# Kernel tuning notes

Measured on AMD Instinct MI355X. Metric: run time of the kernel, lower is better.

## Reference

```python
import jax, jax.numpy as jnp
import numpy as np

M_TIME = 64      # signal model output length (time points)
N_DICT = 20000   # dictionary entries
B_VOX = 8192     # voxels / batch


def setup_inputs() -> dict:
    key = jax.random.key(0)
    k = jax.random.split(key, 6)
    input_real = jax.random.normal(k[0], (M_TIME, B_VOX), jnp.float32)
    input_imag = jax.random.normal(k[1], (M_TIME, B_VOX), jnp.float32)
    # raw dictionary signals, then normalize columns as append() does
    yr = jax.random.normal(k[2], (M_TIME, N_DICT), jnp.float32)
    yi = jax.random.normal(k[3], (M_TIME, N_DICT), jnp.float32)
    norm = jnp.sqrt(jnp.sum(yr * yr + yi * yi, axis=0))  # (N,)
    inverse_norm_y = 1.0 / norm
    y_real = yr * inverse_norm_y
    y_imag = yi * inverse_norm_y
    x_t1 = jax.random.uniform(k[4], (N_DICT,), jnp.float32, 0.1, 3.0)
    x_t2 = jax.random.uniform(k[5], (N_DICT,), jnp.float32, 0.01, 0.5)
    return {
        'input_real': input_real, 'input_imag': input_imag,
        'y_real': y_real, 'y_imag': y_imag,
        'inverse_norm_y': inverse_norm_y, 'x_t1': x_t1, 'x_t2': x_t2,
    }


def reference(input_real, input_imag, y_real, y_imag, inverse_norm_y, x_t1, x_t2):
    # |<y_n, s_b>|^2 for complex y and complex input, via 4 real GEMMs (as in the
    # original module): sim[n, b]
    sim = (jnp.einsum('mb,mn->nb', input_real, y_real) ** 2
           + jnp.einsum('mb,mn->nb', input_real, y_imag) ** 2
           + jnp.einsum('mb,mn->nb', input_imag, y_real) ** 2
           + jnp.einsum('mb,mn->nb', input_imag, y_imag) ** 2)
    idx = jnp.argmax(sim, axis=0)  # (B,)
    # scale = sum_m conj(y[:, idx]) * input * inverse_norm_y[idx]
    yr = y_real[:, idx]   # (M, B)
    yi = y_imag[:, idx]   # (M, B)
    inv = inverse_norm_y[idx]  # (B,)
    scale_r = jnp.sum(yr * input_real + yi * input_imag, axis=0) * inv
    scale_i = jnp.sum(yr * input_imag - yi * input_real, axis=0) * inv
    # returns (scale, t1, t2) with complex scale split into real/imag, stacked (4, B)
    return jnp.stack([scale_r, scale_i, x_t1[idx], x_t2[idx]])
```

## Files before the change

kernel.cpp:

```cpp
#include <hip/hip_runtime.h>
#include <hip/hip_bf16.h>
#include <stdint.h>

#define M_TIME 64
#define N_DICT 20000
#define B_VOX  8192

#define NTILES 313

typedef _Float16 v8h __attribute__((ext_vector_type(8)));
typedef float    v4f __attribute__((ext_vector_type(4)));
typedef float    v2f __attribute__((ext_vector_type(2)));
typedef __attribute__((address_space(3))) unsigned int  lds_u32;
typedef const __attribute__((address_space(1))) unsigned int glb_u32;

__device__ __forceinline__ unsigned long long u64max(unsigned long long a, unsigned long long b) { return a > b ? a : b; }
__device__ __forceinline__ unsigned umin32(unsigned a, unsigned b) { return a < b ? a : b; }
__device__ __forceinline__ unsigned umax32(unsigned a, unsigned b) { return a > b ? a : b; }
__device__ __forceinline__ unsigned umed3(unsigned a, unsigned b, unsigned c) {
    unsigned d;
    asm("v_med3_u32 %0, %1, %2, %3" : "=v"(d) : "v"(a), "v"(b), "v"(c));
    return d;
}

__global__ __launch_bounds__(256) void split_y(
    const float* __restrict__ yr, const float* __restrict__ yi,
    v8h* __restrict__ yp)
{
    const int u = blockIdx.x * 256 + threadIdx.x;
    const int n_l = u & 63;
    const int j   = (u >> 6) & 7;
    const int T   = (u >> 9) % NTILES;
    const int arr = u / (NTILES * 512);
    if (arr > 1) return;
    const float* P = arr ? yi : yr;
    const int n_g = T * 64 + n_l;
    v8h V;
#pragma unroll
    for (int c = 0; c < 8; ++c) {
        float v = 0.f;
        if (n_g < N_DICT) v = P[(j * 8 + c) * N_DICT + n_g];
        V[c] = (_Float16)v;
    }
    const int fr = (arr * 2 + (j >> 2)) * 4 + (j & 3);
    yp[((size_t)T * 16 + fr) * 64 + n_l] = V;
}

__global__ __launch_bounds__(256, 2) void gemm_pre(
    const float* __restrict__ ir, const float* __restrict__ ii,
    const v8h* __restrict__ yp,
    unsigned* __restrict__ cand, int tpc, int slots)
{
    __shared__ float4 ys4[2][1024];
    __shared__ unsigned xm[2][2][16][2];

    const int tid  = threadIdx.x;
    const int wave = tid >> 6, lane = tid & 63;
    const int quad = lane >> 4, col = lane & 15;
    const int wb   = wave >> 1, wn = wave & 1;
    const int vox_w = blockIdx.x * 64 + wb * 32;
    const int chunk = blockIdx.y;
    const int T0 = chunk * tpc;
    const int T1 = (T0 + tpc < NTILES) ? T0 + tpc : NTILES;

    auto dma_tile = [&](int T, int buf) {
        const float4* src = (const float4*)((const char*)yp + (size_t)T * 16384);
#pragma unroll
        for (int p = 0; p < 4; ++p) {
            const int base = p * 256 + wave * 64;
            __builtin_amdgcn_global_load_lds(
                (glb_u32*)(src + base + lane),
                (lds_u32*)(&ys4[buf][base]), 16, 0, 0);
        }
    };

    dma_tile(T0, 0);

    v8h fh[2][2][2];
#pragma unroll
    for (int arr = 0; arr < 2; ++arr) {
        const float* P = arr ? ii : ir;
#pragma unroll
        for (int bt = 0; bt < 2; ++bt) {
            const int b = vox_w + bt * 16 + col;
#pragma unroll
            for (int h = 0; h < 2; ++h) {
                v8h H;
#pragma unroll
                for (int j = 0; j < 8; ++j) {
                    const int k = h * 32 + quad * 8 + j;
                    H[j] = (_Float16)P[k * B_VOX + b];
                }
                fh[arr][bt][h] = H;
            }
        }
    }

    const v4f zc = {0.f, 0.f, 0.f, 0.f};
    unsigned t2a[2] = {0u, 0u}, t2b[2] = {0u, 0u};

    for (int T = T0; T < T1; ++T) {
        const int par = (T - T0) & 1;
        __syncthreads();
        if (T + 1 < T1) dma_tile(T + 1, par ^ 1);
        const v8h* yv = (const v8h*)ys4[par];

        v4f acc[2][2][4];
#pragma unroll
        for (int h = 0; h < 2; ++h) {
#pragma unroll
            for (int nt = 0; nt < 2; ++nt) {
                const int nrow = (wn * 2 + nt) * 16 + col;
                const v8h yfr = yv[((0 * 2 + h) * 4 + quad) * 64 + nrow];
                const v8h yfi = yv[((1 * 2 + h) * 4 + quad) * 64 + nrow];
#pragma unroll
                for (int bt = 0; bt < 2; ++bt) {
#define MF(A, B, C) __builtin_amdgcn_mfma_f32_16x16x32_f16(A, B, C, 0, 0, 0)
                    if (h == 0) {
                        acc[bt][nt][0] = MF(yfr, fh[0][bt][0], zc);
                        acc[bt][nt][1] = MF(yfi, fh[0][bt][0], zc);
                        acc[bt][nt][2] = MF(yfr, fh[1][bt][0], zc);
                        acc[bt][nt][3] = MF(yfi, fh[1][bt][0], zc);
                    } else {
                        acc[bt][nt][0] = MF(yfr, fh[0][bt][1], acc[bt][nt][0]);
                        acc[bt][nt][1] = MF(yfi, fh[0][bt][1], acc[bt][nt][1]);
                        acc[bt][nt][2] = MF(yfr, fh[1][bt][1], acc[bt][nt][2]);
                        acc[bt][nt][3] = MF(yfi, fh[1][bt][1], acc[bt][nt][3]);
                    }
#undef MF
                }
            }
        }

        const int tl = T - T0;
#pragma unroll
        for (int nt = 0; nt < 2; ++nt) {
            const unsigned base = 0x1FFFu
                - (unsigned)(tl * 64 + (wn * 2 + nt) * 16 + quad * 4);
            v2f s01[2], s23[2];
#pragma unroll
            for (int bt = 0; bt < 2; ++bt) {
                const v4f a0 = acc[bt][nt][0], a1 = acc[bt][nt][1];
                const v4f a2 = acc[bt][nt][2], a3 = acc[bt][nt][3];
                {
                    const v2f p0 = __builtin_shufflevector(a0, a0, 0, 1);
                    const v2f p1 = __builtin_shufflevector(a1, a1, 0, 1);
                    const v2f p2 = __builtin_shufflevector(a2, a2, 0, 1);
                    const v2f p3 = __builtin_shufflevector(a3, a3, 0, 1);
                    v2f s = p0 * p0;
                    s = __builtin_elementwise_fma(p1, p1, s);
                    s = __builtin_elementwise_fma(p2, p2, s);
                    s = __builtin_elementwise_fma(p3, p3, s);
                    s01[bt] = s;
                }
                {
                    const v2f p0 = __builtin_shufflevector(a0, a0, 2, 3);
                    const v2f p1 = __builtin_shufflevector(a1, a1, 2, 3);
                    const v2f p2 = __builtin_shufflevector(a2, a2, 2, 3);
                    const v2f p3 = __builtin_shufflevector(a3, a3, 2, 3);
                    v2f s = p0 * p0;
                    s = __builtin_elementwise_fma(p1, p1, s);
                    s = __builtin_elementwise_fma(p2, p2, s);
                    s = __builtin_elementwise_fma(p3, p3, s);
                    s23[bt] = s;
                }
            }
#pragma unroll
            for (int r = 0; r < 4; ++r) {
#pragma unroll
                for (int bt = 0; bt < 2; ++bt) {
                    const float s = (r < 2) ? s01[bt][r] : s23[bt][r - 2];
                    const unsigned pb = (__float_as_uint(s) & 0xFFFFE000u)
                                      | (base - (unsigned)r);
                    const unsigned nb = umed3(pb, t2a[bt], t2b[bt]);
                    t2a[bt] = umax32(pb, t2a[bt]);
                    t2b[bt] = nb;
                }
            }
        }
    }

    unsigned fa1[2], fa2[2];
#pragma unroll
    for (int bt = 0; bt < 2; ++bt) {
        unsigned a1 = t2a[bt], a2 = t2b[bt];
#pragma unroll
        for (int d = 16; d <= 32; d <<= 1) {
            unsigned b1 = (unsigned)__shfl_xor((int)a1, d, 64);
            unsigned b2 = (unsigned)__shfl_xor((int)a2, d, 64);
            unsigned mn = umin32(a1, b1);
            a1 = umax32(a1, b1);
            a2 = umax32(mn, umax32(a2, b2));
        }
        fa1[bt] = a1; fa2[bt] = a2;
    }
    __syncthreads();
    if (wn == 1 && lane < 16) {
#pragma unroll
        for (int bt = 0; bt < 2; ++bt) { xm[wb][bt][lane][0] = fa1[bt]; xm[wb][bt][lane][1] = fa2[bt]; }
    }
    __syncthreads();
    if (wn == 0 && lane < 16) {
#pragma unroll
        for (int bt = 0; bt < 2; ++bt) {
            unsigned b1 = xm[wb][bt][lane][0];
            unsigned b2 = xm[wb][bt][lane][1];
            unsigned m1 = umax32(fa1[bt], b1);
            unsigned m2 = umax32(umin32(fa1[bt], b1), umax32(fa2[bt], b2));
            const size_t vox = vox_w + bt * 16 + lane;
            cand[vox * slots + chunk * 2 + 0] = m1;
            cand[vox * slots + chunk * 2 + 1] = m2;
        }
    }
}

__global__ __launch_bounds__(256) void rescore_finish(
    const float* __restrict__ ir, const float* __restrict__ ii,
    const float* __restrict__ yr, const float* __restrict__ yi,
    const float* __restrict__ inv, const float* __restrict__ x1,
    const float* __restrict__ x2,
    const unsigned* __restrict__ cand, int slots, int tpc,
    float* __restrict__ out)
{
    const int tid  = threadIdx.x;
    const int vox  = blockIdx.x * 4 + (tid >> 6);
    const int slot = tid & 63;

    unsigned p = (slot < slots) ? cand[(size_t)vox * slots + slot] : 0u;
    float sa = __uint_as_float(p & 0xFFFFE000u);
    const int chunkc = slot >> 1;
    const int nn = chunkc * tpc * 64 + (0x1FFF - (int)(p & 0x1FFFu));

    float amax = sa;
#pragma unroll
    for (int d = 1; d <= 32; d <<= 1) amax = fmaxf(amax, __shfl_xor(amax, d, 64));

    unsigned long long q = 0ull;
    float rr = 0.f, ri = 0.f, s1 = 0.f, s2 = 0.f;
    const bool active = (slot < slots) && (nn >= 0) && (nn < N_DICT)
                     && (sa >= 0.97f * amax);
    if (active) {
        for (int m = 0; m < M_TIME; ++m) {
            float a  = yr[(size_t)m * N_DICT + nn];
            float c  = yi[(size_t)m * N_DICT + nn];
            float vr = ir[m * B_VOX + vox];
            float vi = ii[m * B_VOX + vox];
            rr = fmaf(vr, a, rr); ri = fmaf(vr, c, ri);
            s1 = fmaf(vi, a, s1); s2 = fmaf(vi, c, s2);
        }
        float s = fmaf(rr, rr, fmaf(ri, ri, fmaf(s1, s1, s2 * s2)));
        q = (((unsigned long long)__float_as_uint(s)) << 32)
          | (unsigned long long)(0xFFFFFFFFu - (unsigned)nn);
    }
    unsigned long long qm = q;
#pragma unroll
    for (int d = 1; d <= 32; d <<= 1) qm = u64max(qm, __shfl_xor(qm, d, 64));

    if (active && q == qm && qm != 0ull) {
        float ss = inv[nn];
        out[0 * B_VOX + vox] = (rr + s2) * ss;
        out[1 * B_VOX + vox] = (s1 - ri) * ss;
        out[2 * B_VOX + vox] = x1[nn];
        out[3 * B_VOX + vox] = x2[nn];
    }
}

__global__ __launch_bounds__(256, 3) void argmax_naive(
    const float* __restrict__ ir, const float* __restrict__ ii,
    const float* __restrict__ yr, const float* __restrict__ yi,
    int* __restrict__ idxout)
{
    int b = blockIdx.x * 256 + threadIdx.x;
    float bs = -1.0f; int bn = 0;
    for (int n = 0; n < N_DICT; ++n) {
        float a_rr = 0.f, a_ri = 0.f, a_s1 = 0.f, a_s2 = 0.f;
        for (int m = 0; m < M_TIME; ++m) {
            float a = yr[m * N_DICT + n], c = yi[m * N_DICT + n];
            float vr = ir[m * B_VOX + b], vi = ii[m * B_VOX + b];
            a_rr = fmaf(vr, a, a_rr); a_ri = fmaf(vr, c, a_ri);
            a_s1 = fmaf(vi, a, a_s1); a_s2 = fmaf(vi, c, a_s2);
        }
        float sim = fmaf(a_rr, a_rr, fmaf(a_ri, a_ri, fmaf(a_s1, a_s1, a_s2 * a_s2)));
        if (sim > bs) { bs = sim; bn = n; }
    }
    idxout[b] = bn;
}

__global__ void finish_k(const float* __restrict__ ir, const float* __restrict__ ii,
                         const float* __restrict__ yr, const float* __restrict__ yi,
                         const float* __restrict__ inv, const float* __restrict__ x1,
                         const float* __restrict__ x2,
                         const int* __restrict__ idxin, float* __restrict__ out)
{
    int b = blockIdx.x * blockDim.x + threadIdx.x;
    int idx = idxin[b];
    float ar = 0.f, ai = 0.f;
    for (int m = 0; m < M_TIME; ++m) {
        float a  = yr[(size_t)m * N_DICT + idx];
        float c  = yi[(size_t)m * N_DICT + idx];
        float vr = ir[m * B_VOX + b];
        float vi = ii[m * B_VOX + b];
        ar = fmaf(a, vr, ar); ar = fmaf(c, vi, ar);
        ai = fmaf(a, vi, ai); ai = fmaf(-c, vr, ai);
    }
    float s = inv[idx];
    out[0 * B_VOX + b] = ar * s;
    out[1 * B_VOX + b] = ai * s;
    out[2 * B_VOX + b] = x1[idx];
    out[3 * B_VOX + b] = x2[idx];
}

extern "C" void kernel_launch(void* const* d_in, const int* in_sizes, int n_in,
                              void* d_out, int out_size, void* d_ws, size_t ws_size,
                              hipStream_t stream) {
    const float* ir  = (const float*)d_in[0];
    const float* ii  = (const float*)d_in[1];
    const float* yr  = (const float*)d_in[2];
    const float* yi  = (const float*)d_in[3];
    const float* inv = (const float*)d_in[4];
    const float* x1  = (const float*)d_in[5];
    const float* x2  = (const float*)d_in[6];
    float* out = (float*)d_out;

    const size_t yp_bytes = (size_t)NTILES * 16384;

    int CH = 0;
    for (int c = 32; c >= 4; c >>= 1) {
        size_t cand_bytes = (size_t)B_VOX * (2 * c) * sizeof(unsigned);
        if (ws_size >= cand_bytes + yp_bytes) { CH = c; break; }
    }

    if (CH > 0) {
        const int slots = 2 * CH;
        const int tpc   = (NTILES + CH - 1) / CH;
        unsigned* cand = (unsigned*)d_ws;
        v8h* yp = (v8h*)((char*)d_ws + (size_t)B_VOX * slots * sizeof(unsigned));

        const int units = 2 * NTILES * 512;
        split_y<<<(units + 255) / 256, 256, 0, stream>>>(yr, yi, yp);
        gemm_pre<<<dim3(B_VOX / 64, CH), 256, 0, stream>>>(ir, ii, yp, cand, tpc, slots);
        rescore_finish<<<B_VOX / 4, 256, 0, stream>>>(ir, ii, yr, yi, inv, x1, x2,
                                                      cand, slots, tpc, out);
    } else {
        int* idxo = (int*)(out + 3 * B_VOX);
        argmax_naive<<<B_VOX / 256, 256, 0, stream>>>(ir, ii, yr, yi, idxo);
        finish_k<<<B_VOX / 256, 256, 0, stream>>>(ir, ii, yr, yi,
                                                  inv, x1, x2, idxo, out);
    }
}
```

Before: 189.1 us.

## Triple-buffer GEMM tile DMA and add transposed dictionary for rescoring

The GEMM prefetch goes from double to triple buffering. It uses explicit vmcnt waits and a raw barrier, so tile T+2 loads while tile T is computed and one __syncthreads per iteration is dropped. A new trans_y kernel writes the dictionary in an interleaved n-major layout. This lets rescore_finish read each candidate's 64 complex values contiguously instead of with strided column gathers. The costs are an extra kernel launch, about 10 MB more workspace with a fallback when it does not fit, and more LDS per block, which may reduce occupancy.

```diff
diff --git a/kernel.cpp b/kernel.cpp
--- a/kernel.cpp
+++ b/kernel.cpp
@@ -46,12 +46,45 @@
     yp[((size_t)T * 16 + fr) * 64 + n_l] = V;
 }
 
+__global__ __launch_bounds__(256) void trans_y(
+    const float* __restrict__ yr, const float* __restrict__ yi,
+    float2* __restrict__ yt)
+{
+    __shared__ float tr[64][65];
+    __shared__ float ti[64][65];
+    const int t  = threadIdx.x;
+    const int n0 = blockIdx.x * 64;
+    const int nl = t & 63;
+    const int mg = t >> 6;
+    const bool inb = (n0 + nl) < N_DICT;
+#pragma unroll
+    for (int i = 0; i < 16; ++i) {
+        const int m = mg * 16 + i;
+        tr[m][nl] = inb ? yr[m * N_DICT + n0 + nl] : 0.f;
+        ti[m][nl] = inb ? yi[m * N_DICT + n0 + nl] : 0.f;
+    }
+    __syncthreads();
+    const int nw = t >> 2;
+    const int j  = t & 3;
+    if (n0 + nw < N_DICT) {
+        float4* dst = (float4*)(yt + (size_t)(n0 + nw) * 64);
+#pragma unroll
+        for (int k = 0; k < 8; ++k) {
+            const int m = j * 16 + 2 * k;
+            float4 w;
+            w.x = tr[m][nw];     w.y = ti[m][nw];
+            w.z = tr[m + 1][nw]; w.w = ti[m + 1][nw];
+            dst[j * 8 + k] = w;
+        }
+    }
+}
+
 __global__ __launch_bounds__(256, 2) void gemm_pre(
     const float* __restrict__ ir, const float* __restrict__ ii,
     const v8h* __restrict__ yp,
     unsigned* __restrict__ cand, int tpc, int slots)
 {
-    __shared__ float4 ys4[2][1024];
+    __shared__ float4 ys4[3][1024];
     __shared__ unsigned xm[2][2][16][2];
 
     const int tid  = threadIdx.x;
@@ -75,6 +108,7 @@
     };
 
     dma_tile(T0, 0);
+    if (T0 + 1 < T1) dma_tile(T0 + 1, 1);
 
     v8h fh[2][2][2];
 #pragma unroll
@@ -99,11 +133,17 @@
     const v4f zc = {0.f, 0.f, 0.f, 0.f};
     unsigned t2a[2] = {0u, 0u}, t2b[2] = {0u, 0u};
 
+    int cur = 0;
     for (int T = T0; T < T1; ++T) {
-        const int par = (T - T0) & 1;
-        __syncthreads();
-        if (T + 1 < T1) dma_tile(T + 1, par ^ 1);
-        const v8h* yv = (const v8h*)ys4[par];
+        if (T + 1 < T1) asm volatile("s_waitcnt vmcnt(4)" ::: "memory");
+        else            asm volatile("s_waitcnt vmcnt(0)" ::: "memory");
+        __builtin_amdgcn_s_barrier();
+        __builtin_amdgcn_sched_barrier(0);
+        if (T + 2 < T1) {
+            int nb = cur + 2; if (nb >= 3) nb -= 3;
+            dma_tile(T + 2, nb);
+        }
+        const v8h* yv = (const v8h*)ys4[cur];
 
         v4f acc[2][2][4];
 #pragma unroll
@@ -178,6 +218,7 @@
                 }
             }
         }
+        cur = (cur + 1 == 3) ? 0 : cur + 1;
     }
 
     unsigned fa1[2], fa2[2];
@@ -217,6 +258,7 @@
 __global__ __launch_bounds__(256) void rescore_finish(
     const float* __restrict__ ir, const float* __restrict__ ii,
     const float* __restrict__ yr, const float* __restrict__ yi,
+    const float2* __restrict__ yt,
     const float* __restrict__ inv, const float* __restrict__ x1,
     const float* __restrict__ x2,
     const unsigned* __restrict__ cand, int slots, int tpc,
@@ -240,13 +282,27 @@
     const bool active = (slot < slots) && (nn >= 0) && (nn < N_DICT)
                      && (sa >= 0.97f * amax);
     if (active) {
-        for (int m = 0; m < M_TIME; ++m) {
-            float a  = yr[(size_t)m * N_DICT + nn];
-            float c  = yi[(size_t)m * N_DICT + nn];
-            float vr = ir[m * B_VOX + vox];
-            float vi = ii[m * B_VOX + vox];
-            rr = fmaf(vr, a, rr); ri = fmaf(vr, c, ri);
-            s1 = fmaf(vi, a, s1); s2 = fmaf(vi, c, s2);
+        if (yt) {
+            const float4* yc = (const float4*)(yt + (size_t)nn * 64);
+            for (int m2 = 0; m2 < 32; ++m2) {
+                const float4 w = yc[m2];
+                const int m = 2 * m2;
+                float vr0 = ir[m * B_VOX + vox],       vi0 = ii[m * B_VOX + vox];
+                float vr1 = ir[(m + 1) * B_VOX + vox], vi1 = ii[(m + 1) * B_VOX + vox];
+                rr = fmaf(vr0, w.x, rr); ri = fmaf(vr0, w.y, ri);
+                s1 = fmaf(vi0, w.x, s1); s2 = fmaf(vi0, w.y, s2);
+                rr = fmaf(vr1, w.z, rr); ri = fmaf(vr1, w.w, ri);
+                s1 = fmaf(vi1, w.z, s1); s2 = fmaf(vi1, w.w, s2);
+            }
+        } else {
+            for (int m = 0; m < M_TIME; ++m) {
+                float a  = yr[(size_t)m * N_DICT + nn];
+                float c  = yi[(size_t)m * N_DICT + nn];
+                float vr = ir[m * B_VOX + vox];
+                float vi = ii[m * B_VOX + vox];
+                rr = fmaf(vr, a, rr); ri = fmaf(vr, c, ri);
+                s1 = fmaf(vi, a, s1); s2 = fmaf(vi, c, s2);
+            }
         }
         float s = fmaf(rr, rr, fmaf(ri, ri, fmaf(s1, s1, s2 * s2)));
         q = (((unsigned long long)__float_as_uint(s)) << 32)
@@ -323,11 +379,18 @@
     float* out = (float*)d_out;
 
     const size_t yp_bytes = (size_t)NTILES * 16384;
-
-    int CH = 0;
+    const size_t yt_bytes = (size_t)N_DICT * 64 * sizeof(float2);
+
+    int CH = 0; bool use_yt = false;
     for (int c = 32; c >= 4; c >>= 1) {
         size_t cand_bytes = (size_t)B_VOX * (2 * c) * sizeof(unsigned);
-        if (ws_size >= cand_bytes + yp_bytes) { CH = c; break; }
+        if (ws_size >= cand_bytes + yp_bytes + yt_bytes) { CH = c; use_yt = true; break; }
+    }
+    if (CH == 0) {
+        for (int c = 32; c >= 4; c >>= 1) {
+            size_t cand_bytes = (size_t)B_VOX * (2 * c) * sizeof(unsigned);
+            if (ws_size >= cand_bytes + yp_bytes) { CH = c; break; }
+        }
     }
 
     if (CH > 0) {
@@ -335,11 +398,13 @@
         const int tpc   = (NTILES + CH - 1) / CH;
         unsigned* cand = (unsigned*)d_ws;
         v8h* yp = (v8h*)((char*)d_ws + (size_t)B_VOX * slots * sizeof(unsigned));
+        float2* yt = use_yt ? (float2*)((char*)yp + yp_bytes) : nullptr;
 
         const int units = 2 * NTILES * 512;
         split_y<<<(units + 255) / 256, 256, 0, stream>>>(yr, yi, yp);
+        if (use_yt) trans_y<<<NTILES, 256, 0, stream>>>(yr, yi, yt);
         gemm_pre<<<dim3(B_VOX / 64, CH), 256, 0, stream>>>(ir, ii, yp, cand, tpc, slots);
-        rescore_finish<<<B_VOX / 4, 256, 0, stream>>>(ir, ii, yr, yi, inv, x1, x2,
+        rescore_finish<<<B_VOX / 4, 256, 0, stream>>>(ir, ii, yr, yi, yt, inv, x1, x2,
                                                       cand, slots, tpc, out);
     } else {
         int* idxo = (int*)(out + 3 * B_VOX);
```

Result: slower. 201.3 us (+6.5%).

## Load dictionary fragments directly from global into registers, drop LDS double buffer

Applied to the files above, without the earlier changes.

Replaces the LDS double-buffered DMA of each dictionary tile (global_load_lds plus a block barrier per tile) with per-wave direct global loads of the MFMA operand fragments into registers, prefetched one tile ahead. This removes the __syncthreads per tile and the LDS traffic, letting waves proceed independently. The cost is more global/L2 traffic, since the two voxel waves sharing the same dictionary rows now each fetch them, plus extra registers for the prefetched fragments, which could lower occupancy.

```diff
diff --git a/kernel.cpp b/kernel.cpp
--- a/kernel.cpp
+++ b/kernel.cpp
@@ -11,8 +11,6 @@
 typedef _Float16 v8h __attribute__((ext_vector_type(8)));
 typedef float    v4f __attribute__((ext_vector_type(4)));
 typedef float    v2f __attribute__((ext_vector_type(2)));
-typedef __attribute__((address_space(3))) unsigned int  lds_u32;
-typedef const __attribute__((address_space(1))) unsigned int glb_u32;
 
 __device__ __forceinline__ unsigned long long u64max(unsigned long long a, unsigned long long b) { return a > b ? a : b; }
 __device__ __forceinline__ unsigned umin32(unsigned a, unsigned b) { return a < b ? a : b; }
@@ -51,7 +49,6 @@
     const v8h* __restrict__ yp,
     unsigned* __restrict__ cand, int tpc, int slots)
 {
-    __shared__ float4 ys4[2][1024];
     __shared__ unsigned xm[2][2][16][2];
 
     const int tid  = threadIdx.x;
@@ -63,19 +60,6 @@
     const int T0 = chunk * tpc;
     const int T1 = (T0 + tpc < NTILES) ? T0 + tpc : NTILES;
 
-    auto dma_tile = [&](int T, int buf) {
-        const float4* src = (const float4*)((const char*)yp + (size_t)T * 16384);
-#pragma unroll
-        for (int p = 0; p < 4; ++p) {
-            const int base = p * 256 + wave * 64;
-            __builtin_amdgcn_global_load_lds(
-                (glb_u32*)(src + base + lane),
-                (lds_u32*)(&ys4[buf][base]), 16, 0, 0);
-        }
-    };
-
-    dma_tile(T0, 0);
-
     v8h fh[2][2][2];
 #pragma unroll
     for (int arr = 0; arr < 2; ++arr) {
@@ -96,41 +80,49 @@
         }
     }
 
+    v8h yfr[2][2], yfi[2][2];
+    auto loadf = [&](int T) {
+        const v8h* yv = (const v8h*)((const char*)yp + (size_t)T * 16384);
+#pragma unroll
+        for (int h = 0; h < 2; ++h)
+#pragma unroll
+            for (int nt = 0; nt < 2; ++nt) {
+                const int nrow = (wn * 2 + nt) * 16 + col;
+                yfr[h][nt] = yv[((0 * 2 + h) * 4 + quad) * 64 + nrow];
+                yfi[h][nt] = yv[((1 * 2 + h) * 4 + quad) * 64 + nrow];
+            }
+    };
+
     const v4f zc = {0.f, 0.f, 0.f, 0.f};
     unsigned t2a[2] = {0u, 0u}, t2b[2] = {0u, 0u};
 
+    loadf(T0);
     for (int T = T0; T < T1; ++T) {
-        const int par = (T - T0) & 1;
-        __syncthreads();
-        if (T + 1 < T1) dma_tile(T + 1, par ^ 1);
-        const v8h* yv = (const v8h*)ys4[par];
-
         v4f acc[2][2][4];
 #pragma unroll
         for (int h = 0; h < 2; ++h) {
 #pragma unroll
             for (int nt = 0; nt < 2; ++nt) {
-                const int nrow = (wn * 2 + nt) * 16 + col;
-                const v8h yfr = yv[((0 * 2 + h) * 4 + quad) * 64 + nrow];
-                const v8h yfi = yv[((1 * 2 + h) * 4 + quad) * 64 + nrow];
 #pragma unroll
                 for (int bt = 0; bt < 2; ++bt) {
 #define MF(A, B, C) __builtin_amdgcn_mfma_f32_16x16x32_f16(A, B, C, 0, 0, 0)
                     if (h == 0) {
-                        acc[bt][nt][0] = MF(yfr, fh[0][bt][0], zc);
-                        acc[bt][nt][1] = MF(yfi, fh[0][bt][0], zc);
-                        acc[bt][nt][2] = MF(yfr, fh[1][bt][0], zc);
-                        acc[bt][nt][3] = MF(yfi, fh[1][bt][0], zc);
+                        acc[bt][nt][0] = MF(yfr[0][nt], fh[0][bt][0], zc);
+                        acc[bt][nt][1] = MF(yfi[0][nt], fh[0][bt][0], zc);
+                        acc[bt][nt][2] = MF(yfr[0][nt], fh[1][bt][0], zc);
+                        acc[bt][nt][3] = MF(yfi[0][nt], fh[1][bt][0], zc);
                     } else {
-                        acc[bt][nt][0] = MF(yfr, fh[0][bt][1], acc[bt][nt][0]);
-                        acc[bt][nt][1] = MF(yfi, fh[0][bt][1], acc[bt][nt][1]);
-                        acc[bt][nt][2] = MF(yfr, fh[1][bt][1], acc[bt][nt][2]);
-                        acc[bt][nt][3] = MF(yfi, fh[1][bt][1], acc[bt][nt][3]);
+                        acc[bt][nt][0] = MF(yfr[1][nt], fh[0][bt][1], acc[bt][nt][0]);
+                        acc[bt][nt][1] = MF(yfi[1][nt], fh[0][bt][1], acc[bt][nt][1]);
+                        acc[bt][nt][2] = MF(yfr[1][nt], fh[1][bt][1], acc[bt][nt][2]);
+                        acc[bt][nt][3] = MF(yfi[1][nt], fh[1][bt][1], acc[bt][nt][3]);
                     }
 #undef MF
                 }
             }
         }
+
+        if (T + 1 < T1) loadf(T + 1);
 
         const int tl = T - T0;
 #pragma unroll
```

New measurement: 188.1 us. About the same (-0.5%).
